# Kernel optimization log

Measured on AMD Instinct MI355X. Metric: run time of the kernel, lower is better.

## Reference

```python
import jax, jax.numpy as jnp
import numpy as np

S = 24; N = S * S; D = 1024; B = 4; H = 8; HD = D // H; K = 8
LN_EPS = 1e-5


def _spiral_indices(s, clockwise):
    inds = []
    top, bottom, left, right = 0, s - 1, 0, s - 1
    if clockwise:
        while top <= bottom and left <= right:
            for j in range(left, right + 1):
                inds.append((top, j))
            top += 1
            for i in range(top, bottom + 1):
                inds.append((i, right))
            right -= 1
            if top <= bottom:
                for j in range(right, left - 1, -1):
                    inds.append((bottom, j))
                bottom -= 1
            if left <= right:
                for i in range(bottom, top - 1, -1):
                    inds.append((i, left))
                left += 1
    else:
        while top <= bottom and left <= right:
            for i in range(top, bottom + 1):
                inds.append((i, left))
            left += 1
            for j in range(left, right + 1):
                inds.append((bottom, j))
            bottom -= 1
            if left <= right:
                for i in range(bottom, top - 1, -1):
                    inds.append((i, right))
                right -= 1
            if top <= bottom:
                for j in range(right, left - 1, -1):
                    inds.append((top, j))
                top += 1
    return np.array([i * s + j for i, j in inds], dtype=np.int32)


def _diag_indices(s, anti):
    idx = []
    for offset in (range(2 * s - 1) if anti else range(-(s - 1), s)):
        for i in range(s):
            j = (offset - i) if anti else (i + offset)
            if 0 <= j < s:
                idx.append(i * s + j)
    return np.array(idx, dtype=np.int32)


def _build_scan_indices(s):
    # Composite (scan + restore) permutation per direction: out_i = Linear_i(x[:, idx_i])
    ar = np.arange(s * s, dtype=np.int32).reshape(s, s)
    lr = ar.reshape(-1)                      # left_right: identity
    rl_scan = ar[:, ::-1].reshape(-1)        # right_left scan
    rl_restore = ar[:, ::-1].reshape(-1)     # restore flips width back
    rl = rl_scan[rl_restore]                 # composes to identity
    tb = ar.T.reshape(-1)                    # top_bottom (restore is plain view -> no inverse!)
    bt_scan = ar[::-1, :].T.reshape(-1)      # bottom_top scan: flip(transpose) flatten
    bt_restore = ar[::-1, :].reshape(-1)     # restore: view->transpose->flip(2)->transpose
    bt = bt_scan[bt_restore]
    dm = _diag_indices(s, anti=False)        # restore is plain view
    da = _diag_indices(s, anti=True)
    sc = _spiral_indices(s, clockwise=True)
    scc = _spiral_indices(s, clockwise=False)
    return np.stack([lr, rl, tb, bt, dm, da, sc, scc], axis=0)  # [8, N]


def setup_inputs() -> dict:
    key = jax.random.key(0)
    ks = jax.random.split(key, 12)
    sc = D ** -0.5
    return {
        "vision_features": jax.random.normal(ks[0], (B, N, D), dtype=jnp.float32),
        "dir_W": jax.random.normal(ks[1], (K, D, D), dtype=jnp.float32) * sc,
        "dir_b": jax.random.normal(ks[2], (K, D), dtype=jnp.float32) * 0.01,
        "in_proj_w": jax.random.normal(ks[3], (3 * D, D), dtype=jnp.float32) * sc,
        "in_proj_b": jax.random.normal(ks[4], (3 * D,), dtype=jnp.float32) * 0.01,
        "out_proj_w": jax.random.normal(ks[5], (D, D), dtype=jnp.float32) * sc,
        "out_proj_b": jax.random.normal(ks[6], (D,), dtype=jnp.float32) * 0.01,
        "fin_w": jax.random.normal(ks[7], (D, D), dtype=jnp.float32) * sc,
        "fin_b": jax.random.normal(ks[8], (D,), dtype=jnp.float32) * 0.01,
        "ln_g": jnp.ones((D,), dtype=jnp.float32),
        "ln_b": jnp.zeros((D,), dtype=jnp.float32),
        "scan_idx": jnp.asarray(_build_scan_indices(S)),  # [8, N] int32
    }


def reference(vision_features, dir_W, dir_b, in_proj_w, in_proj_b,
              out_proj_w, out_proj_b, fin_w, fin_b, ln_g, ln_b, scan_idx):
    b, n, d = vision_features.shape
    # Fused per-direction gather + batched GEMM: [B,8,N,D]
    gathered = vision_features[:, scan_idx]                     # [B,K,N,D]
    dirs = jnp.einsum('bknd,kde->bkne', gathered, dir_W) + dir_b[None, :, None, :]
    kv = dirs.reshape(b, K * n, d)                              # [B,8N,D]
    # MultiheadAttention (batch_first, 8 heads, eval -> no dropout)
    wq, wk, wv = in_proj_w[:d], in_proj_w[d:2 * d], in_proj_w[2 * d:]
    bq, bk, bv = in_proj_b[:d], in_proj_b[d:2 * d], in_proj_b[2 * d:]
    q = (vision_features @ wq.T + bq).reshape(b, n, H, HD).transpose(0, 2, 1, 3)
    k = (kv @ wk.T + bk).reshape(b, K * n, H, HD).transpose(0, 2, 1, 3)
    v = (kv @ wv.T + bv).reshape(b, K * n, H, HD).transpose(0, 2, 1, 3)
    scores = jnp.einsum('bhnd,bhmd->bhnm', q, k) / jnp.sqrt(jnp.asarray(HD, q.dtype))
    attn = jax.nn.softmax(scores, axis=-1)
    o = jnp.einsum('bhnm,bhmd->bhnd', attn, v).transpose(0, 2, 1, 3).reshape(b, n, d)
    fused = o @ out_proj_w.T + out_proj_b
    # output_projection: Linear -> LayerNorm (dropout inactive)
    y = fused @ fin_w.T + fin_b
    mu = jnp.mean(y, axis=-1, keepdims=True)
    var = jnp.mean(jnp.square(y - mu), axis=-1, keepdims=True)
    y = (y - mu) * jax.lax.rsqrt(var + LN_EPS) * ln_g + ln_b
    return y + vision_features
```

## Files before the change

### kernel.cpp

```cpp
#include <hip/hip_runtime.h>
#include <hip/hip_bf16.h>

typedef __attribute__((ext_vector_type(8))) short short8;
typedef __attribute__((ext_vector_type(4))) float f32x4;
typedef __attribute__((ext_vector_type(4))) int i32x4;

#define NTOK 576
#define DIM  1024
#define NB   4
#define NH   8
#define HD   128
#define KDIR 8
#define KN   4608
#define NSPLIT 4
#define NT 18

__device__ __forceinline__ float us2f(unsigned short u) {
    unsigned int x = ((unsigned int)u) << 16;
    return __uint_as_float(x);
}
__device__ __forceinline__ unsigned short f2us(float f) {
    unsigned int x = __float_as_uint(f);
    unsigned int r = x + 0x7fffu + ((x >> 16) & 1u);
    return (unsigned short)(r >> 16);
}

typedef __attribute__((address_space(3))) unsigned int lds_uint;
typedef const __attribute__((address_space(1))) unsigned int glb_uint;
__device__ __forceinline__ void async16(const unsigned short* g, unsigned short* l) {
    __builtin_amdgcn_global_load_lds((glb_uint*)g, (lds_uint*)l, 16, 0, 0);
}
__device__ __forceinline__ void wait_vm0_barrier() {
    asm volatile("s_waitcnt vmcnt(0)" ::: "memory");
    __builtin_amdgcn_s_barrier();
    __builtin_amdgcn_sched_barrier(0);
}

__global__ void detect_kernel(const unsigned int* __restrict__ src, int* meta)
{
    if (threadIdx.x == 0) {
        int cnt = 0;
        for (int i = 0; i < 256; ++i) {
            unsigned u = src[(long)i * 16384] & 0xFFFFu;
            unsigned e = (u >> 7) & 0xFFu;
            cnt += (e >= 90 && e <= 150) ? 1 : 0;
        }
        meta[0] = (cnt >= 192) ? 1 : 0;
    }
}

struct ConvJobs {
    const void* src[10];
    unsigned short* dst[10];
    int n4[10];
    int bstart[10];
};
__global__ __launch_bounds__(256)
void conv_all(ConvJobs J, const int* __restrict__ meta)
{
    const int b = blockIdx.x;
    int ji = 0;
    #pragma unroll
    for (int i = 1; i < 10; ++i) if (b >= J.bstart[i]) ji = i;
    const long base = (long)(b - J.bstart[ji]) * 1024 + threadIdx.x;
    const long n4 = J.n4[ji];
    if (meta[0]) {
        const ushort4* s = (const ushort4*)J.src[ji];
        ushort4* d = (ushort4*)J.dst[ji];
        #pragma unroll
        for (int t = 0; t < 4; ++t) {
            long i = base + t * 256;
            if (i < n4) d[i] = s[i];
        }
    } else {
        const float4* s = (const float4*)J.src[ji];
        ushort4* d = (ushort4*)J.dst[ji];
        #pragma unroll
        for (int t = 0; t < 4; ++t) {
            long i = base + t * 256;
            if (i < n4) {
                float4 v = s[i];
                ushort4 o;
                o.x = f2us(v.x); o.y = f2us(v.y); o.z = f2us(v.z); o.w = f2us(v.w);
                d[i] = o;
            }
        }
    }
}

__global__ __launch_bounds__(256)
void transpose_conv(const void* __restrict__ src, unsigned short* __restrict__ dst,
                    const int* __restrict__ meta)
{
    const int k = blockIdx.y;
    const int ty = blockIdx.x >> 5, tx = blockIdx.x & 31;
    const int d0 = ty * 32, e0 = tx * 32;
    __shared__ float tl[32][33];
    const int t = threadIdx.x;
    const int row = t >> 3, c4 = (t & 7) * 4;
    const long sbase = ((long)k * 1024 + d0 + row) * 1024 + e0 + c4;
    if (meta[0]) {
        const unsigned short* s = (const unsigned short*)src;
        ushort4 v = *(const ushort4*)(s + sbase);
        tl[row][c4+0] = us2f(v.x); tl[row][c4+1] = us2f(v.y);
        tl[row][c4+2] = us2f(v.z); tl[row][c4+3] = us2f(v.w);
    } else {
        const float* s = (const float*)src;
        float4 v = *(const float4*)(s + sbase);
        tl[row][c4+0] = v.x; tl[row][c4+1] = v.y;
        tl[row][c4+2] = v.z; tl[row][c4+3] = v.w;
    }
    __syncthreads();
    ushort4 o;
    o.x = f2us(tl[c4+0][row]); o.y = f2us(tl[c4+1][row]);
    o.z = f2us(tl[c4+2][row]); o.w = f2us(tl[c4+3][row]);
    *(ushort4*)(dst + ((long)k * 1024 + e0 + row) * 1024 + d0 + c4) = o;
}

template<int MODE, int TN, int BM, int BN>
__global__ __launch_bounds__(256)
void gemm_glds(const unsigned short* __restrict__ A, const unsigned short* __restrict__ Bw,
               const unsigned short* __restrict__ bias, unsigned short* __restrict__ C,
               const unsigned short* __restrict__ B2, const unsigned short* __restrict__ bias2,
               unsigned short* __restrict__ C2,
               int M, long bStride, long biasStride)
{
    constexpr int MI = BM / 32, NI = BN / 32;
    const int z = blockIdx.y;
    const unsigned short* Bb;
    const unsigned short* Gb;
    if constexpr (MODE == 6) {
        Bb = (z < 8) ? Bw + (long)z * bStride : B2;
        Gb = (z < 8) ? bias + (long)z * biasStride : bias2;
    } else {
        Bb = Bw + (long)z * bStride;
        Gb = bias + (long)z * biasStride;
    }
    const int tm = blockIdx.x / TN;
    const int tn = blockIdx.x % TN;

    __shared__ __align__(16) unsigned short As[BM * 64];
    __shared__ __align__(16) unsigned short Bs[BN * 64];

    const int tid = threadIdx.x, lane = tid & 63, wid = tid >> 6;
    const int wm = wid >> 1, wn = wid & 1;
    const int r0 = lane & 15, hi = lane >> 4;
    const int lr = lane >> 3;
    const int lg = lane & 7;

    f32x4 zz = {0.f, 0.f, 0.f, 0.f};
    f32x4 acc[MI][NI];
    #pragma unroll
    for (int i = 0; i < MI; ++i)
        #pragma unroll
        for (int j = 0; j < NI; ++j) acc[i][j] = zz;

    const int sgc = ((lg ^ (lr & 7)) << 3);

    for (int k0 = 0; k0 < 1024; k0 += 64) {
        #pragma unroll
        for (int j = 0; j < BM / 32; ++j) {
            int rb = wid * (BM / 4) + j * 8;
            async16(A + (long)(tm * BM + rb + lr) * 1024 + k0 + sgc, &As[rb * 64]);
        }
        #pragma unroll
        for (int j = 0; j < BN / 32; ++j) {
            int rb = wid * (BN / 4) + j * 8;
            async16(Bb + (long)(tn * BN + rb + lr) * 1024 + k0 + sgc, &Bs[rb * 64]);
        }
        __syncthreads();
        __builtin_amdgcn_s_setprio(1);
        #pragma unroll
        for (int kd = 0; kd < 2; ++kd) {
            const int pg = ((kd * 4 + hi) ^ (r0 & 7)) << 3;
            short8 af[MI], bfr[NI];
            #pragma unroll
            for (int mi = 0; mi < MI; ++mi)
                af[mi] = *reinterpret_cast<const short8*>(&As[(wm * (BM/2) + mi * 16 + r0) * 64 + pg]);
            #pragma unroll
            for (int ni = 0; ni < NI; ++ni)
                bfr[ni] = *reinterpret_cast<const short8*>(&Bs[(wn * (BN/2) + ni * 16 + r0) * 64 + pg]);
            #pragma unroll
            for (int mi = 0; mi < MI; ++mi)
                #pragma unroll
                for (int ni = 0; ni < NI; ++ni)
                    acc[mi][ni] = __builtin_amdgcn_mfma_f32_16x16x32_bf16(af[mi], bfr[ni], acc[mi][ni], 0, 0, 0);
        }
        __builtin_amdgcn_s_setprio(0);
        __syncthreads();
    }

    const float QSCL = 0.08838834764831845f * 1.4426950408889634f;
    const int jr = hi * 4;
    #pragma unroll
    for (int ni = 0; ni < NI; ++ni) {
        int cg = tn * BN + wn * (BN/2) + ni * 16 + r0;
        float bv = us2f(Gb[cg]);
        if constexpr (MODE == 5) {
            if (cg >= 1024) {
                int cg2 = cg - 1024;
                int h = cg2 >> 7, d = cg2 & 127;
                #pragma unroll
                for (int mi = 0; mi < MI; ++mi) {
                    int rgb = tm * BM + wm * (BM/2) + mi * 16 + jr;
                    int b = rgb / 4608, kv = rgb - b * 4608;
                    int r = kv & 63;
                    int P = ((r >> 5) & 1) * 32 + ((r >> 3) & 1) * 16 + ((r >> 2) & 1) * 8
                          + ((r >> 4) & 1) * 4 + (r & 3);
                    ushort4 o;
                    o.x = f2us(acc[mi][ni][0] + bv);
                    o.y = f2us(acc[mi][ni][1] + bv);
                    o.z = f2us(acc[mi][ni][2] + bv);
                    o.w = f2us(acc[mi][ni][3] + bv);
                    *(ushort4*)&C2[((long)(b * 8 + h) * 128 + d) * 4608 + (kv & ~63) + P] = o;
                }
                continue;
            }
        }
        #pragma unroll
        for (int mi = 0; mi < MI; ++mi) {
            #pragma unroll
            for (int j = 0; j < 4; ++j) {
                int rg = tm * BM + wm * (BM/2) + mi * 16 + jr + j;
                float val = acc[mi][ni][j] + bv;
                if constexpr (MODE == 0) {
                    C[(long)rg * 1024 + cg] = f2us(val);
                } else if constexpr (MODE == 5) {
                    int b = rg / 4608, kv = rg - b * 4608;
                    int h = cg >> 7, d = cg & 127;
                    C[((long)(b * 8 + h) * 4608 + kv) * 128 + d] = f2us(val);
                } else {
                    int b = rg / 576, n = rg - b * 576;
                    if (z == 8) {
                        int h = cg >> 7, d = cg & 127;
                        C2[((long)(b * 8 + h) * 576 + n) * 128 + d] = f2us(val * QSCL);
                    } else {
                        C[((long)b * 4608 + (long)z * 576 + n) * 1024 + cg] = f2us(val);
                    }
                }
            }
        }
    }
}

__global__ __launch_bounds__(256, 2)
void attn_kernel7(const unsigned short* __restrict__ Qh, const unsigned short* __restrict__ Kh,
                  const unsigned short* __restrict__ VTh, unsigned short* __restrict__ Opart,
                  float2* __restrict__ Ml)
{
    const int bid = blockIdx.x;
    const int logical = (bid & 7) * 48 + (bid >> 3);
    const int bhsp = logical / 3;
    const int qt = logical - bhsp * 3;
    const int bh = bhsp >> 2;
    const int sp = bhsp & 3;

    const int tid = threadIdx.x;
    const int lane = tid & 63, wid = tid >> 6;
    const int r0 = lane & 15, hi = lane >> 4;

    __shared__ __align__(16) unsigned short Ks[2][64 * 128];
    __shared__ __align__(16) unsigned short VT[2][128 * 64];

    short8 qf[3][4];
    #pragma unroll
    for (int c = 0; c < 3; ++c) {
        const long qoff = ((long)bh * NTOK + qt * 192 + c * 64 + wid * 16 + r0) * HD + hi * 8;
        #pragma unroll
        for (int kd = 0; kd < 4; ++kd)
            qf[c][kd] = *reinterpret_cast<const short8*>(Qh + qoff + kd * 32);
    }

    f32x4 zz = {0.f, 0.f, 0.f, 0.f};
    f32x4 oacc[3][8];
    #pragma unroll
    for (int c = 0; c < 3; ++c)
        #pragma unroll
        for (int i = 0; i < 8; ++i) oacc[c][i] = zz;
    float mrun[3], lrun[3];
    #pragma unroll
    for (int c = 0; c < 3; ++c) { mrun[c] = -1e30f; lrun[c] = 0.f; }

    int offK[4], offV[4];
    #pragma unroll
    for (int j = 0; j < 4; ++j) {
        offK[j] = (wid * 16 + 4 * j + hi) * 128 + (((lane & 15) ^ ((4 * j + hi) & 7)) << 3);
        offV[j] = (wid * 32 + 8 * j + (lane >> 3)) * KN + (((lane & 7) ^ (lane >> 3)) << 3);
    }
    const unsigned short* kp = Kh + (long)bh * KN * HD + (long)(sp * (KN / NSPLIT)) * HD;
    const unsigned short* vp = VTh + (long)bh * HD * KN + sp * (KN / NSPLIT);

    auto stage = [&](int buf) {
        #pragma unroll
        for (int j = 0; j < 4; ++j) {
            async16(kp + offK[j], &Ks[buf][(wid * 16 + 4 * j) * 128]);
            async16(vp + offV[j], &VT[buf][(wid * 32 + 8 * j) * 64]);
        }
    };

    stage(0);
    for (int kt = 0; kt < NT; ++kt) {
        wait_vm0_barrier();
        if (kt < NT - 1) { kp += 64 * HD; vp += 64; stage((kt + 1) & 1); }
        const unsigned short* Ksb = Ks[kt & 1];
        const unsigned short* VTb = VT[kt & 1];

        f32x4 s[3][4];
        #pragma unroll
        for (int c = 0; c < 3; ++c)
            #pragma unroll
            for (int nb = 0; nb < 4; ++nb) s[c][nb] = zz;
        __builtin_amdgcn_s_setprio(1);
        #pragma unroll
        for (int nb = 0; nb < 4; ++nb) {
            #pragma unroll
            for (int kd = 0; kd < 4; ++kd) {
                short8 kf = *reinterpret_cast<const short8*>(
                    &Ksb[(nb * 16 + r0) * 128 + (((kd * 4 + hi) ^ (r0 & 7)) << 3)]);
                s[0][nb] = __builtin_amdgcn_mfma_f32_16x16x32_bf16(kf, qf[0][kd], s[0][nb], 0, 0, 0);
                s[1][nb] = __builtin_amdgcn_mfma_f32_16x16x32_bf16(kf, qf[1][kd], s[1][nb], 0, 0, 0);
                s[2][nb] = __builtin_amdgcn_mfma_f32_16x16x32_bf16(kf, qf[2][kd], s[2][nb], 0, 0, 0);
            }
        }
        __builtin_amdgcn_s_setprio(0);

        unsigned pk0[3][4], pk1[3][4];
        #pragma unroll
        for (int c = 0; c < 3; ++c) {
            float mt = fmaxf(fmaxf(fmaxf(s[c][0][0], s[c][0][1]), fmaxf(s[c][0][2], s[c][0][3])),
                       fmaxf(fmaxf(fmaxf(s[c][1][0], s[c][1][1]), fmaxf(s[c][1][2], s[c][1][3])),
                       fmaxf(fmaxf(fmaxf(s[c][2][0], s[c][2][1]), fmaxf(s[c][2][2], s[c][2][3])),
                             fmaxf(fmaxf(s[c][3][0], s[c][3][1]), fmaxf(s[c][3][2], s[c][3][3])))));
            if (!__all(mt - mrun[c] <= 8.0f)) {
                float mr = fmaxf(mt, __shfl_xor(mt, 16));
                mr = fmaxf(mr, __shfl_xor(mr, 32));
                float mn = fmaxf(mrun[c], mr);
                float scl = exp2f(mrun[c] - mn);
                mrun[c] = mn;
                lrun[c] *= scl;
                #pragma unroll
                for (int db = 0; db < 8; ++db)
                    #pragma unroll
                    for (int j = 0; j < 4; ++j)
                        oacc[c][db][j] *= scl;
            }
            float rt = 0.f;
            #pragma unroll
            for (int nb = 0; nb < 4; ++nb)
                #pragma unroll
                for (int j = 0; j < 4; ++j) {
                    s[c][nb][j] = exp2f(s[c][nb][j] - mrun[c]);
                    rt += s[c][nb][j];
                }
            lrun[c] += rt;
            #pragma unroll
            for (int nb = 0; nb < 4; ++nb) {
                asm("v_cvt_pk_bf16_f32 %0, %1, %2" : "=v"(pk0[c][nb]) : "v"(s[c][nb][0]), "v"(s[c][nb][1]));
                asm("v_cvt_pk_bf16_f32 %0, %1, %2" : "=v"(pk1[c][nb]) : "v"(s[c][nb][2]), "v"(s[c][nb][3]));
            }
        }

        __builtin_amdgcn_s_setprio(1);
        #pragma unroll
        for (int kd = 0; kd < 2; ++kd) {
            short8 pf[3];
            #pragma unroll
            for (int c = 0; c < 3; ++c) {
                i32x4 fr;
                fr[0] = (int)pk0[c][2 * kd];
                fr[1] = (int)pk1[c][2 * kd];
                fr[2] = (int)pk0[c][2 * kd + 1];
                fr[3] = (int)pk1[c][2 * kd + 1];
                pf[c] = *reinterpret_cast<short8*>(&fr);
            }
            #pragma unroll
            for (int db = 0; db < 8; ++db) {
                short8 vf = *reinterpret_cast<const short8*>(
                    &VTb[(db * 16 + r0) * 64 + (((kd * 4 + hi) ^ (r0 & 7)) << 3)]);
                oacc[0][db] = __builtin_amdgcn_mfma_f32_16x16x32_bf16(vf, pf[0], oacc[0][db], 0, 0, 0);
                oacc[1][db] = __builtin_amdgcn_mfma_f32_16x16x32_bf16(vf, pf[1], oacc[1][db], 0, 0, 0);
                oacc[2][db] = __builtin_amdgcn_mfma_f32_16x16x32_bf16(vf, pf[2], oacc[2][db], 0, 0, 0);
            }
        }
        __builtin_amdgcn_s_setprio(0);
    }

    #pragma unroll
    for (int c = 0; c < 3; ++c) {
        float lr = lrun[c];
        lr += __shfl_xor(lr, 16);
        lr += __shfl_xor(lr, 32);
        const float inv = 1.f / lr;
        const long po = ((long)(sp * 32 + bh) * NTOK + qt * 192 + c * 64 + wid * 16 + r0) * HD;
        #pragma unroll
        for (int db = 0; db < 8; ++db) {
            ushort4 o;
            o.x = f2us(oacc[c][db][0] * inv);
            o.y = f2us(oacc[c][db][1] * inv);
            o.z = f2us(oacc[c][db][2] * inv);
            o.w = f2us(oacc[c][db][3] * inv);
            *(ushort4*)&Opart[po + db * 16 + hi * 4] = o;
        }
        if (lane < 16) {
            const long mo = (long)(sp * 32 + bh) * NTOK + qt * 192 + c * 64 + wid * 16 + r0;
            Ml[mo] = make_float2(mrun[c], lr);
        }
    }
}

__global__ __launch_bounds__(256)
void attn_reduce(const unsigned short* __restrict__ Opart, const float2* __restrict__ Ml,
                 unsigned short* __restrict__ Ob)
{
    const int qt = blockIdx.x, bh = blockIdx.y;
    const int t = threadIdx.x;
    const int rl = t >> 2, dc = (t & 3) * 32;
    const int q = qt * 64 + rl;

    float m[NSPLIT], l[NSPLIT];
    float M = -1e30f;
    #pragma unroll
    for (int sp = 0; sp < NSPLIT; ++sp) {
        float2 v = Ml[(long)(sp * 32 + bh) * NTOK + q];
        m[sp] = v.x; l[sp] = v.y;
        M = fmaxf(M, v.x);
    }
    float w[NSPLIT], denom = 0.f;
    #pragma unroll
    for (int sp = 0; sp < NSPLIT; ++sp) {
        w[sp] = l[sp] * exp2f(m[sp] - M);
        denom += w[sp];
    }
    const float inv = 1.f / denom;
    const int b = bh >> 3, h = bh & 7;
    #pragma unroll
    for (int dj = 0; dj < 4; ++dj) {
        float a[8];
        #pragma unroll
        for (int e = 0; e < 8; ++e) a[e] = 0.f;
        #pragma unroll
        for (int sp = 0; sp < NSPLIT; ++sp) {
            short8 v = *reinterpret_cast<const short8*>(
                &Opart[((long)(sp * 32 + bh) * NTOK + q) * HD + dc + dj * 8]);
            #pragma unroll
            for (int e = 0; e < 8; ++e)
                a[e] += w[sp] * us2f((unsigned short)v[e]);
        }
        short8 o;
        #pragma unroll
        for (int e = 0; e < 8; ++e) o[e] = (short)f2us(a[e] * inv);
        *reinterpret_cast<short8*>(&Ob[((long)b * NTOK + q) * 1024 + h * 128 + dc + dj * 8]) = o;
    }
}

__global__ __launch_bounds__(256)
void ln2_kernel(const unsigned short* __restrict__ Y, const unsigned short* __restrict__ g,
                const unsigned short* __restrict__ be, const unsigned short* __restrict__ vis,
                void* __restrict__ dout, const int* __restrict__ meta)
{
    const int row = blockIdx.x;
    const int tid = threadIdx.x;
    const int lane = tid & 63, wid = tid >> 6;
    const unsigned short* yr = Y + (long)row * DIM;
    ushort4 raw = reinterpret_cast<const ushort4*>(yr)[tid];
    float v[4];
    v[0] = us2f(raw.x); v[1] = us2f(raw.y); v[2] = us2f(raw.z); v[3] = us2f(raw.w);
    float s1 = 0.f, s2 = 0.f;
    #pragma unroll
    for (int i = 0; i < 4; ++i) { s1 += v[i]; s2 += v[i] * v[i]; }
    #pragma unroll
    for (int off = 1; off < 64; off <<= 1) {
        s1 += __shfl_xor(s1, off);
        s2 += __shfl_xor(s2, off);
    }
    __shared__ float red[2][4];
    if (lane == 0) { red[0][wid] = s1; red[1][wid] = s2; }
    __syncthreads();
    s1 = red[0][0] + red[0][1] + red[0][2] + red[0][3];
    s2 = red[1][0] + red[1][1] + red[1][2] + red[1][3];
    const float mu = s1 * (1.f / DIM);
    const float var = s2 * (1.f / DIM) - mu * mu;
    const float inv = rsqrtf(var + 1e-5f);
    ushort4 gg = reinterpret_cast<const ushort4*>(g)[tid];
    ushort4 bb = reinterpret_cast<const ushort4*>(be)[tid];
    ushort4 vv = reinterpret_cast<const ushort4*>(vis + (long)row * DIM)[tid];
    float o0 = (v[0] - mu) * inv * us2f(gg.x) + us2f(bb.x) + us2f(vv.x);
    float o1 = (v[1] - mu) * inv * us2f(gg.y) + us2f(bb.y) + us2f(vv.y);
    float o2 = (v[2] - mu) * inv * us2f(gg.z) + us2f(bb.z) + us2f(vv.z);
    float o3 = (v[3] - mu) * inv * us2f(gg.w) + us2f(bb.w) + us2f(vv.w);
    if (meta[0]) {
        ushort4 o;
        o.x = f2us(o0); o.y = f2us(o1); o.z = f2us(o2); o.w = f2us(o3);
        reinterpret_cast<ushort4*>((unsigned short*)dout + (long)row * DIM)[tid] = o;
    } else {
        float4 o = make_float4(o0, o1, o2, o3);
        reinterpret_cast<float4*>((float*)dout + (long)row * DIM)[tid] = o;
    }
}

extern "C" void kernel_launch(void* const* d_in, const int* in_sizes, int n_in,
                              void* d_out, int out_size, void* d_ws, size_t ws_size,
                              hipStream_t stream)
{
    unsigned long long w = (unsigned long long)d_ws;
    int* meta = (int*)w; w += 256;

    const int cidx[10] = {0, 2, 3, 4, 5, 6, 7, 8, 9, 10};
    const long csz[10] = {
        (long)NB * NTOK * DIM,
        (long)KDIR * DIM,
        3L * DIM * DIM,
        3L * DIM,
        (long)DIM * DIM,
        DIM,
        (long)DIM * DIM,
        DIM, DIM, DIM
    };
    unsigned short* cv[10];
    for (int i = 0; i < 10; ++i) {
        cv[i] = (unsigned short*)w;
        w += (csz[i] * 2 + 255) & ~255ULL;
    }
    unsigned short* dWT = (unsigned short*)w; w += (long)KDIR * DIM * DIM * 2;

    const size_t big = (size_t)NB * KDIR * NTOK * DIM * 2;
    const size_t sml = (size_t)NB * NTOK * DIM * 2;
    unsigned short* dirs = (unsigned short*)w; w += big;
    unsigned short* Kh   = (unsigned short*)w; w += big;
    unsigned short* VTh  = (unsigned short*)w; w += big;
    unsigned short* Qh   = (unsigned short*)w; w += sml;
    unsigned short* Ob   = (unsigned short*)w; w += sml;
    unsigned short* Fu   = (unsigned short*)w; w += sml;
    unsigned short* Y2   = (unsigned short*)w; w += sml;
    float2* Ml = (float2*)w; w += (long)NSPLIT * 32 * NTOK * sizeof(float2);
    unsigned short* Opart = dirs;

    const unsigned short* vision = cv[0];
    const unsigned short* dirb = cv[1];
    const unsigned short* inW = cv[2];
    const unsigned short* inB = cv[3];
    const unsigned short* outW = cv[4];
    const unsigned short* outB = cv[5];
    const unsigned short* finW = cv[6];
    const unsigned short* finB = cv[7];
    const unsigned short* lng = cv[8];
    const unsigned short* lnbt = cv[9];

    dim3 blk(256, 1, 1);

    detect_kernel<<<dim3(1), dim3(64), 0, stream>>>((const unsigned int*)d_in[1], meta);

    ConvJobs J;
    int bacc = 0;
    for (int i = 0; i < 10; ++i) {
        J.src[i] = d_in[cidx[i]];
        J.dst[i] = cv[i];
        J.n4[i] = (int)(csz[i] / 4);
        J.bstart[i] = bacc;
        bacc += (int)((csz[i] / 4 + 1023) / 1024);
    }
    conv_all<<<dim3(bacc), blk, 0, stream>>>(J, meta);
    transpose_conv<<<dim3(1024, KDIR), blk, 0, stream>>>(d_in[1], dWT, meta);

    gemm_glds<6, 8, 128, 128><<<dim3(18 * 8, 9), blk, 0, stream>>>(
        vision, dWT, dirb, dirs, inW, inB, Qh, NB * NTOK, (long)DIM * DIM, DIM);

    gemm_glds<5, 16, 128, 128><<<dim3(144 * 16, 1), blk, 0, stream>>>(
        dirs, inW + DIM * DIM, inB + DIM, Kh, nullptr, nullptr, VTh, NB * KN, 0L, 0L);

    attn_kernel7<<<dim3(3 * 32 * NSPLIT), blk, 0, stream>>>(Qh, Kh, VTh, Opart, Ml);

    attn_reduce<<<dim3(9, 32), blk, 0, stream>>>(Opart, Ml, Ob);

    gemm_glds<0, 16, 64, 64><<<dim3(36 * 16, 1), blk, 0, stream>>>(
        Ob, outW, outB, Fu, nullptr, nullptr, nullptr, NB * NTOK, 0L, 0L);

    gemm_glds<0, 16, 64, 64><<<dim3(36 * 16, 1), blk, 0, stream>>>(
        Fu, finW, finB, Y2, nullptr, nullptr, nullptr, NB * NTOK, 0L, 0L);

    ln2_kernel<<<dim3(NB * NTOK), blk, 0, stream>>>(Y2, lng, lnbt, vision, d_out, meta);
}
```

Baseline: 332.3 us.

## Add dedicated 256x256-tile K/V projection GEMM with 8-wave double-buffered pipeline

```diff
diff --git a/kernel.cpp b/kernel.cpp
--- a/kernel.cpp
+++ b/kernel.cpp
@@ -196,27 +196,6 @@
     for (int ni = 0; ni < NI; ++ni) {
         int cg = tn * BN + wn * (BN/2) + ni * 16 + r0;
         float bv = us2f(Gb[cg]);
-        if constexpr (MODE == 5) {
-            if (cg >= 1024) {
-                int cg2 = cg - 1024;
-                int h = cg2 >> 7, d = cg2 & 127;
-                #pragma unroll
-                for (int mi = 0; mi < MI; ++mi) {
-                    int rgb = tm * BM + wm * (BM/2) + mi * 16 + jr;
-                    int b = rgb / 4608, kv = rgb - b * 4608;
-                    int r = kv & 63;
-                    int P = ((r >> 5) & 1) * 32 + ((r >> 3) & 1) * 16 + ((r >> 2) & 1) * 8
-                          + ((r >> 4) & 1) * 4 + (r & 3);
-                    ushort4 o;
-                    o.x = f2us(acc[mi][ni][0] + bv);
-                    o.y = f2us(acc[mi][ni][1] + bv);
-                    o.z = f2us(acc[mi][ni][2] + bv);
-                    o.w = f2us(acc[mi][ni][3] + bv);
-                    *(ushort4*)&C2[((long)(b * 8 + h) * 128 + d) * 4608 + (kv & ~63) + P] = o;
-                }
-                continue;
-            }
-        }
         #pragma unroll
         for (int mi = 0; mi < MI; ++mi) {
             #pragma unroll
@@ -225,10 +204,6 @@
                 float val = acc[mi][ni][j] + bv;
                 if constexpr (MODE == 0) {
                     C[(long)rg * 1024 + cg] = f2us(val);
-                } else if constexpr (MODE == 5) {
-                    int b = rg / 4608, kv = rg - b * 4608;
-                    int h = cg >> 7, d = cg & 127;
-                    C[((long)(b * 8 + h) * 4608 + kv) * 128 + d] = f2us(val);
                 } else {
                     int b = rg / 576, n = rg - b * 576;
                     if (z == 8) {
@@ -238,6 +213,136 @@
                         C[((long)b * 4608 + (long)z * 576 + n) * 1024 + cg] = f2us(val);
                     }
                 }
+            }
+        }
+    }
+}
+
+__global__ __launch_bounds__(512, 1)
+void gemm_kv8(const unsigned short* __restrict__ A, const unsigned short* __restrict__ Bw,
+              const unsigned short* __restrict__ bias, unsigned short* __restrict__ Kh,
+              unsigned short* __restrict__ VTh)
+{
+    const int tm = blockIdx.x >> 3;
+    const int tn = blockIdx.x & 7;
+
+    __shared__ __align__(16) unsigned short As[2][256 * 64];
+    __shared__ __align__(16) unsigned short Bs[2][256 * 64];
+
+    const int tid = threadIdx.x, lane = tid & 63, wid = tid >> 6;
+    const int wm = wid >> 2, wn = wid & 3;
+    const int r0 = lane & 15, hi = lane >> 4;
+
+    const int srow = tid >> 3;
+    const int sgc  = (((tid & 7) ^ (srow & 7)) << 3);
+    const long abase = (long)(tm * 256 + srow) * 1024 + sgc;
+    const long bbase = (long)(tn * 256 + srow) * 1024 + sgc;
+    const int  ldst  = wid * 512;
+
+    f32x4 zz = {0.f, 0.f, 0.f, 0.f};
+    f32x4 acc[8][4];
+    #pragma unroll
+    for (int i = 0; i < 8; ++i)
+        #pragma unroll
+        for (int j = 0; j < 4; ++j) acc[i][j] = zz;
+
+    auto stageA = [&](int kt, int buf) {
+        #pragma unroll
+        for (int r = 0; r < 4; ++r)
+            async16(A + abase + (long)r * 65536 + kt * 64, &As[buf][r * 4096 + ldst]);
+    };
+    auto stageB = [&](int kt, int buf) {
+        #pragma unroll
+        for (int r = 0; r < 4; ++r)
+            async16(Bw + bbase + (long)r * 65536 + kt * 64, &Bs[buf][r * 4096 + ldst]);
+    };
+
+    stageA(0, 0);
+    stageB(0, 0);
+
+    const int arow0 = wm * 128 + r0;
+    const int brow0 = wn * 64 + r0;
+    const int pg0 = ((hi ^ (r0 & 7)) << 3);
+    const int pg1 = (((4 + hi) ^ (r0 & 7)) << 3);
+
+    for (int kt = 0; kt < 16; ++kt) {
+        const unsigned short* Ac = As[kt & 1];
+        const unsigned short* Bc = Bs[kt & 1];
+        __builtin_amdgcn_s_barrier();
+        if (kt < 15) {
+            stageA(kt + 1, (kt + 1) & 1);
+            asm volatile("s_waitcnt vmcnt(4)" ::: "memory");
+        } else {
+            asm volatile("s_waitcnt vmcnt(0)" ::: "memory");
+        }
+        __builtin_amdgcn_sched_barrier(0);
+
+        #pragma unroll
+        for (int q = 0; q < 4; ++q) {
+            if (q == 1 && kt < 15) stageB(kt + 1, (kt + 1) & 1);
+            short8 af[2][2], bf[4][2];
+            #pragma unroll
+            for (int dm = 0; dm < 2; ++dm) {
+                const int row = (arow0 + (q * 2 + dm) * 16) * 64;
+                af[dm][0] = *reinterpret_cast<const short8*>(&Ac[row + pg0]);
+                af[dm][1] = *reinterpret_cast<const short8*>(&Ac[row + pg1]);
+            }
+            #pragma unroll
+            for (int ni = 0; ni < 4; ++ni) {
+                const int row = (brow0 + ni * 16) * 64;
+                bf[ni][0] = *reinterpret_cast<const short8*>(&Bc[row + pg0]);
+                bf[ni][1] = *reinterpret_cast<const short8*>(&Bc[row + pg1]);
+            }
+            __builtin_amdgcn_s_setprio(1);
+            #pragma unroll
+            for (int dm = 0; dm < 2; ++dm)
+                #pragma unroll
+                for (int ni = 0; ni < 4; ++ni) {
+                    acc[q*2+dm][ni] = __builtin_amdgcn_mfma_f32_16x16x32_bf16(af[dm][0], bf[ni][0], acc[q*2+dm][ni], 0, 0, 0);
+                    acc[q*2+dm][ni] = __builtin_amdgcn_mfma_f32_16x16x32_bf16(af[dm][1], bf[ni][1], acc[q*2+dm][ni], 0, 0, 0);
+                }
+            __builtin_amdgcn_s_setprio(0);
+            __builtin_amdgcn_sched_barrier(0);
+        }
+    }
+
+    const int jr = hi * 4;
+    if (tn < 4) {
+        #pragma unroll
+        for (int ni = 0; ni < 4; ++ni) {
+            int cg = tn * 256 + wn * 64 + ni * 16 + r0;
+            float bv = us2f(bias[cg]);
+            int h = cg >> 7, d = cg & 127;
+            #pragma unroll
+            for (int mi = 0; mi < 8; ++mi) {
+                #pragma unroll
+                for (int j = 0; j < 4; ++j) {
+                    int rg = tm * 256 + wm * 128 + mi * 16 + jr + j;
+                    int b = rg / 4608, kv = rg - b * 4608;
+                    Kh[((long)(b * 8 + h) * 4608 + kv) * 128 + d] = f2us(acc[mi][ni][j] + bv);
+                }
+            }
+        }
+    } else {
+        #pragma unroll
+        for (int ni = 0; ni < 4; ++ni) {
+            int cgr = tn * 256 + wn * 64 + ni * 16 + r0;
+            float bv = us2f(bias[cgr]);
+            int cg = cgr - 1024;
+            int h = cg >> 7, d = cg & 127;
+            #pragma unroll
+            for (int mi = 0; mi < 8; ++mi) {
+                int rgb = tm * 256 + wm * 128 + mi * 16 + jr;
+                int b = rgb / 4608, kv = rgb - b * 4608;
+                int r = kv & 63;
+                int P = ((r >> 5) & 1) * 32 + ((r >> 3) & 1) * 16 + ((r >> 2) & 1) * 8
+                      + ((r >> 4) & 1) * 4 + (r & 3);
+                ushort4 o;
+                o.x = f2us(acc[mi][ni][0] + bv);
+                o.y = f2us(acc[mi][ni][1] + bv);
+                o.z = f2us(acc[mi][ni][2] + bv);
+                o.w = f2us(acc[mi][ni][3] + bv);
+                *(ushort4*)&VTh[((long)(b * 8 + h) * 128 + d) * 4608 + (kv & ~63) + P] = o;
             }
         }
     }
@@ -565,8 +670,8 @@
     gemm_glds<6, 8, 128, 128><<<dim3(18 * 8, 9), blk, 0, stream>>>(
         vision, dWT, dirb, dirs, inW, inB, Qh, NB * NTOK, (long)DIM * DIM, DIM);
 
-    gemm_glds<5, 16, 128, 128><<<dim3(144 * 16, 1), blk, 0, stream>>>(
-        dirs, inW + DIM * DIM, inB + DIM, Kh, nullptr, nullptr, VTh, NB * KN, 0L, 0L);
+    gemm_kv8<<<dim3(72 * 8), dim3(512), 0, stream>>>(
+        dirs, inW + DIM * DIM, inB + DIM, Kh, VTh);
 
     attn_kernel7<<<dim3(3 * 32 * NSPLIT), blk, 0, stream>>>(Qh, Kh, VTh, Opart, Ml);
 
```

After: 366.0 us. +10.1%, slower.

## Fold direction linear into K/V projection weights to skip dirs intermediate

Applied to the files above, without the earlier changes.

```diff
diff --git a/kernel.cpp b/kernel.cpp
--- a/kernel.cpp
+++ b/kernel.cpp
@@ -50,10 +50,10 @@
 }
 
 struct ConvJobs {
-    const void* src[10];
-    unsigned short* dst[10];
-    int n4[10];
-    int bstart[10];
+    const void* src[11];
+    unsigned short* dst[11];
+    int n4[11];
+    int bstart[11];
 };
 __global__ __launch_bounds__(256)
 void conv_all(ConvJobs J, const int* __restrict__ meta)
@@ -61,7 +61,7 @@
     const int b = blockIdx.x;
     int ji = 0;
     #pragma unroll
-    for (int i = 1; i < 10; ++i) if (b >= J.bstart[i]) ji = i;
+    for (int i = 1; i < 11; ++i) if (b >= J.bstart[i]) ji = i;
     const long base = (long)(b - J.bstart[ji]) * 1024 + threadIdx.x;
     const long n4 = J.n4[ji];
     if (meta[0]) {
@@ -89,32 +89,25 @@
 }
 
 __global__ __launch_bounds__(256)
-void transpose_conv(const void* __restrict__ src, unsigned short* __restrict__ dst,
-                    const int* __restrict__ meta)
-{
-    const int k = blockIdx.y;
-    const int ty = blockIdx.x >> 5, tx = blockIdx.x & 31;
-    const int d0 = ty * 32, e0 = tx * 32;
-    __shared__ float tl[32][33];
-    const int t = threadIdx.x;
-    const int row = t >> 3, c4 = (t & 7) * 4;
-    const long sbase = ((long)k * 1024 + d0 + row) * 1024 + e0 + c4;
-    if (meta[0]) {
-        const unsigned short* s = (const unsigned short*)src;
-        ushort4 v = *(const ushort4*)(s + sbase);
-        tl[row][c4+0] = us2f(v.x); tl[row][c4+1] = us2f(v.y);
-        tl[row][c4+2] = us2f(v.z); tl[row][c4+3] = us2f(v.w);
-    } else {
-        const float* s = (const float*)src;
-        float4 v = *(const float4*)(s + sbase);
-        tl[row][c4+0] = v.x; tl[row][c4+1] = v.y;
-        tl[row][c4+2] = v.z; tl[row][c4+3] = v.w;
-    }
-    __syncthreads();
-    ushort4 o;
-    o.x = f2us(tl[c4+0][row]); o.y = f2us(tl[c4+1][row]);
-    o.z = f2us(tl[c4+2][row]); o.w = f2us(tl[c4+3][row]);
-    *(ushort4*)(dst + ((long)k * 1024 + e0 + row) * 1024 + d0 + c4) = o;
+void bias_fold(const unsigned short* __restrict__ dirb, const unsigned short* __restrict__ wkv,
+               const unsigned short* __restrict__ inbkv, unsigned short* __restrict__ bkv)
+{
+    const int w4 = threadIdx.x >> 6, lane = threadIdx.x & 63;
+    const int p = blockIdx.x * 4 + w4;
+    const int z = p >> 11, j = p & 2047;
+    const unsigned short* a = dirb + z * 1024 + lane * 16;
+    const unsigned short* b = wkv + (long)j * 1024 + lane * 16;
+    short8 av0 = *(const short8*)a, av1 = *(const short8*)(a + 8);
+    short8 bv0 = *(const short8*)b, bv1 = *(const short8*)(b + 8);
+    float s = 0.f;
+    #pragma unroll
+    for (int e = 0; e < 8; ++e) {
+        s += us2f((unsigned short)av0[e]) * us2f((unsigned short)bv0[e]);
+        s += us2f((unsigned short)av1[e]) * us2f((unsigned short)bv1[e]);
+    }
+    #pragma unroll
+    for (int off = 1; off < 64; off <<= 1) s += __shfl_xor(s, off);
+    if (lane == 0) bkv[p] = f2us(s + us2f(inbkv[j]));
 }
 
 template<int MODE, int TN, int BM, int BN>
@@ -122,22 +115,24 @@
 void gemm_glds(const unsigned short* __restrict__ A, const unsigned short* __restrict__ Bw,
                const unsigned short* __restrict__ bias, unsigned short* __restrict__ C,
                const unsigned short* __restrict__ B2, const unsigned short* __restrict__ bias2,
-               unsigned short* __restrict__ C2,
-               int M, long bStride, long biasStride)
+               unsigned short* __restrict__ C2, unsigned short* __restrict__ C3,
+               int M, long aStride, long bStride, long biasStride)
 {
     constexpr int MI = BM / 32, NI = BN / 32;
     const int z = blockIdx.y;
+    const int tm = blockIdx.x / TN;
+    const int tn = blockIdx.x % TN;
+    const unsigned short* Ab = A + (long)z * aStride;
     const unsigned short* Bb;
     const unsigned short* Gb;
-    if constexpr (MODE == 6) {
+    if constexpr (MODE == 8) {
+        if (z == 8 && tn >= 8) return;
         Bb = (z < 8) ? Bw + (long)z * bStride : B2;
         Gb = (z < 8) ? bias + (long)z * biasStride : bias2;
     } else {
         Bb = Bw + (long)z * bStride;
         Gb = bias + (long)z * biasStride;
     }
-    const int tm = blockIdx.x / TN;
-    const int tn = blockIdx.x % TN;
 
     __shared__ __align__(16) unsigned short As[BM * 64];
     __shared__ __align__(16) unsigned short Bs[BN * 64];
@@ -161,7 +156,7 @@
         #pragma unroll
         for (int j = 0; j < BM / 32; ++j) {
             int rb = wid * (BM / 4) + j * 8;
-            async16(A + (long)(tm * BM + rb + lr) * 1024 + k0 + sgc, &As[rb * 64]);
+            async16(Ab + (long)(tm * BM + rb + lr) * 1024 + k0 + sgc, &As[rb * 64]);
         }
         #pragma unroll
         for (int j = 0; j < BN / 32; ++j) {
@@ -195,15 +190,38 @@
     #pragma unroll
     for (int ni = 0; ni < NI; ++ni) {
         int cg = tn * BN + wn * (BN/2) + ni * 16 + r0;
-        float bv = us2f(Gb[cg]);
-        if constexpr (MODE == 5) {
-            if (cg >= 1024) {
+        if constexpr (MODE == 7) {
+            #pragma unroll
+            for (int mi = 0; mi < MI; ++mi) {
+                int rg = tm * BM + wm * (BM/2) + mi * 16 + jr;
+                ushort4 o;
+                o.x = f2us(acc[mi][ni][0]);
+                o.y = f2us(acc[mi][ni][1]);
+                o.z = f2us(acc[mi][ni][2]);
+                o.w = f2us(acc[mi][ni][3]);
+                *(ushort4*)&C[((long)z * 2048 + cg) * 1024 + rg] = o;
+            }
+        } else if constexpr (MODE == 8) {
+            float bv = us2f(Gb[cg]);
+            if (z == 8) {
+                int h = cg >> 7, d = cg & 127;
+                #pragma unroll
+                for (int mi = 0; mi < MI; ++mi) {
+                    #pragma unroll
+                    for (int j = 0; j < 4; ++j) {
+                        int rg = tm * BM + wm * (BM/2) + mi * 16 + jr + j;
+                        int b = rg / 576, n = rg - b * 576;
+                        C3[((long)(b * 8 + h) * 576 + n) * 128 + d] = f2us((acc[mi][ni][j] + bv) * QSCL);
+                    }
+                }
+            } else if (cg >= 1024) {
                 int cg2 = cg - 1024;
                 int h = cg2 >> 7, d = cg2 & 127;
                 #pragma unroll
                 for (int mi = 0; mi < MI; ++mi) {
                     int rgb = tm * BM + wm * (BM/2) + mi * 16 + jr;
-                    int b = rgb / 4608, kv = rgb - b * 4608;
+                    int b = rgb / 576, n = rgb - b * 576;
+                    int kv = z * 576 + n;
                     int r = kv & 63;
                     int P = ((r >> 5) & 1) * 32 + ((r >> 3) & 1) * 16 + ((r >> 2) & 1) * 8
                           + ((r >> 4) & 1) * 4 + (r & 3);
@@ -214,29 +232,27 @@
                     o.w = f2us(acc[mi][ni][3] + bv);
                     *(ushort4*)&C2[((long)(b * 8 + h) * 128 + d) * 4608 + (kv & ~63) + P] = o;
                 }
-                continue;
-            }
-        }
-        #pragma unroll
-        for (int mi = 0; mi < MI; ++mi) {
-            #pragma unroll
-            for (int j = 0; j < 4; ++j) {
-                int rg = tm * BM + wm * (BM/2) + mi * 16 + jr + j;
-                float val = acc[mi][ni][j] + bv;
-                if constexpr (MODE == 0) {
-                    C[(long)rg * 1024 + cg] = f2us(val);
-                } else if constexpr (MODE == 5) {
-                    int b = rg / 4608, kv = rg - b * 4608;
-                    int h = cg >> 7, d = cg & 127;
-                    C[((long)(b * 8 + h) * 4608 + kv) * 128 + d] = f2us(val);
-                } else {
-                    int b = rg / 576, n = rg - b * 576;
-                    if (z == 8) {
-                        int h = cg >> 7, d = cg & 127;
-                        C2[((long)(b * 8 + h) * 576 + n) * 128 + d] = f2us(val * QSCL);
-                    } else {
-                        C[((long)b * 4608 + (long)z * 576 + n) * 1024 + cg] = f2us(val);
+            } else {
+                int h = cg >> 7, d = cg & 127;
+                #pragma unroll
+                for (int mi = 0; mi < MI; ++mi) {
+                    #pragma unroll
+                    for (int j = 0; j < 4; ++j) {
+                        int rg = tm * BM + wm * (BM/2) + mi * 16 + jr + j;
+                        int b = rg / 576, n = rg - b * 576;
+                        int kv = z * 576 + n;
+                        C[((long)(b * 8 + h) * 4608 + kv) * 128 + d] = f2us(acc[mi][ni][j] + bv);
                     }
+                }
+            }
+        } else {
+            float bv = us2f(Gb[cg]);
+            #pragma unroll
+            for (int mi = 0; mi < MI; ++mi) {
+                #pragma unroll
+                for (int j = 0; j < 4; ++j) {
+                    int rg = tm * BM + wm * (BM/2) + mi * 16 + jr + j;
+                    C[(long)rg * 1024 + cg] = f2us(acc[mi][ni][j] + bv);
                 }
             }
         }
@@ -505,8 +521,8 @@
     unsigned long long w = (unsigned long long)d_ws;
     int* meta = (int*)w; w += 256;
 
-    const int cidx[10] = {0, 2, 3, 4, 5, 6, 7, 8, 9, 10};
-    const long csz[10] = {
+    const int cidx[11] = {0, 2, 3, 4, 5, 6, 7, 8, 9, 10, 1};
+    const long csz[11] = {
         (long)NB * NTOK * DIM,
         (long)KDIR * DIM,
         3L * DIM * DIM,
@@ -514,18 +530,19 @@
         (long)DIM * DIM,
         DIM,
         (long)DIM * DIM,
-        DIM, DIM, DIM
+        DIM, DIM, DIM,
+        (long)KDIR * DIM * DIM
     };
-    unsigned short* cv[10];
-    for (int i = 0; i < 10; ++i) {
+    unsigned short* cv[11];
+    for (int i = 0; i < 11; ++i) {
         cv[i] = (unsigned short*)w;
         w += (csz[i] * 2 + 255) & ~255ULL;
     }
-    unsigned short* dWT = (unsigned short*)w; w += (long)KDIR * DIM * DIM * 2;
+    unsigned short* dirWb = cv[10];
 
     const size_t big = (size_t)NB * KDIR * NTOK * DIM * 2;
     const size_t sml = (size_t)NB * NTOK * DIM * 2;
-    unsigned short* dirs = (unsigned short*)w; w += big;
+    unsigned short* Fkv = (unsigned short*)w; w += (long)KDIR * 2048 * 1024 * 2;
     unsigned short* Kh   = (unsigned short*)w; w += big;
     unsigned short* VTh  = (unsigned short*)w; w += big;
     unsigned short* Qh   = (unsigned short*)w; w += sml;
@@ -533,7 +550,8 @@
     unsigned short* Fu   = (unsigned short*)w; w += sml;
     unsigned short* Y2   = (unsigned short*)w; w += sml;
     float2* Ml = (float2*)w; w += (long)NSPLIT * 32 * NTOK * sizeof(float2);
-    unsigned short* Opart = dirs;
+    unsigned short* bkv = (unsigned short*)w; w += KDIR * 2048 * 2 + 256;
+    unsigned short* Opart = Fkv;
 
     const unsigned short* vision = cv[0];
     const unsigned short* dirb = cv[1];
@@ -552,7 +570,7 @@
 
     ConvJobs J;
     int bacc = 0;
-    for (int i = 0; i < 10; ++i) {
+    for (int i = 0; i < 11; ++i) {
         J.src[i] = d_in[cidx[i]];
         J.dst[i] = cv[i];
         J.n4[i] = (int)(csz[i] / 4);
@@ -560,23 +578,26 @@
         bacc += (int)((csz[i] / 4 + 1023) / 1024);
     }
     conv_all<<<dim3(bacc), blk, 0, stream>>>(J, meta);
-    transpose_conv<<<dim3(1024, KDIR), blk, 0, stream>>>(d_in[1], dWT, meta);
-
-    gemm_glds<6, 8, 128, 128><<<dim3(18 * 8, 9), blk, 0, stream>>>(
-        vision, dWT, dirb, dirs, inW, inB, Qh, NB * NTOK, (long)DIM * DIM, DIM);
-
-    gemm_glds<5, 16, 128, 128><<<dim3(144 * 16, 1), blk, 0, stream>>>(
-        dirs, inW + DIM * DIM, inB + DIM, Kh, nullptr, nullptr, VTh, NB * KN, 0L, 0L);
+
+    gemm_glds<7, 16, 128, 128><<<dim3(8 * 16, 8), blk, 0, stream>>>(
+        dirWb, inW + DIM * DIM, nullptr, Fkv, nullptr, nullptr, nullptr, nullptr,
+        1024, (long)DIM * DIM, 0L, 0L);
+
+    bias_fold<<<dim3(4096), blk, 0, stream>>>(dirb, inW + DIM * DIM, inB + DIM, bkv);
+
+    gemm_glds<8, 16, 128, 128><<<dim3(18 * 16, 9), blk, 0, stream>>>(
+        vision, Fkv, bkv, Kh, inW, inB, VTh, Qh,
+        NB * NTOK, 0L, (long)2048 * 1024, 2048L);
 
     attn_kernel7<<<dim3(3 * 32 * NSPLIT), blk, 0, stream>>>(Qh, Kh, VTh, Opart, Ml);
 
     attn_reduce<<<dim3(9, 32), blk, 0, stream>>>(Opart, Ml, Ob);
 
     gemm_glds<0, 16, 64, 64><<<dim3(36 * 16, 1), blk, 0, stream>>>(
-        Ob, outW, outB, Fu, nullptr, nullptr, nullptr, NB * NTOK, 0L, 0L);
+        Ob, outW, outB, Fu, nullptr, nullptr, nullptr, nullptr, NB * NTOK, 0L, 0L, 0L);
 
     gemm_glds<0, 16, 64, 64><<<dim3(36 * 16, 1), blk, 0, stream>>>(
-        Fu, finW, finB, Y2, nullptr, nullptr, nullptr, NB * NTOK, 0L, 0L);
+        Fu, finW, finB, Y2, nullptr, nullptr, nullptr, nullptr, NB * NTOK, 0L, 0L, 0L);
 
     ln2_kernel<<<dim3(NB * NTOK), blk, 0, stream>>>(Y2, lng, lnbt, vision, d_out, meta);
 }
```

Measured after the change: 344.7 us. 1.04x slower.
